# Optimization experiments

Measured on AMD Instinct MI355X. Metric: run time of the kernel, lower is better.

Reference implementation:

```python
import jax, jax.numpy as jnp
import numpy as np

B, S, D, H = 2, 2048, 1024, 16
HD = D // H


def setup_inputs() -> dict:
    key = jax.random.key(0)
    ks = jax.random.split(key, 7)
    mk = lambda k, shape, scale=1.0: (jax.random.normal(k, shape, dtype=jnp.float32) * scale)
    w_scale = 1.0 / np.sqrt(D)  # ~nn.Linear init scale
    return {
        "query": mk(ks[0], (B, S, D)),
        "key": mk(ks[1], (B, S, D)),
        "value": mk(ks[2], (B, S, D)),
        "Wq": mk(ks[3], (D, D), w_scale),
        "Wk": mk(ks[4], (D, D), w_scale),
        "Wv": mk(ks[5], (D, D), w_scale),
        "Wo": mk(ks[6], (D, D), w_scale),
    }


def reference(query, key, value, Wq, Wk, Wv, Wo):
    # torch nn.Linear(bias=False): y = x @ W.T, W is (out, in)
    def proj(x, W):
        y = jnp.einsum('bsd,ed->bse', x, W)          # [B, S, D]
        return y.reshape(x.shape[0], x.shape[1], H, HD).transpose(0, 2, 1, 3)  # [B, H, S, HD]

    Q = proj(query, Wq)
    K = proj(key, Wk)
    V = proj(value, Wv)

    # NOTE: original scales by sqrt(embedding_size), not sqrt(head_dim)
    scale = 1.0 / jnp.sqrt(jnp.asarray(D, dtype=Q.dtype))
    scores = jnp.einsum('bhqd,bhkd->bhqk', Q, K) * scale   # [B, H, Q, K]
    attn = jax.nn.softmax(scores, axis=-1)
    ctx = jnp.einsum('bhqk,bhkd->bhqd', attn, V)           # [B, H, Q, HD]
    ctx = ctx.transpose(0, 2, 1, 3).reshape(query.shape[0], query.shape[1], D)
    return jnp.einsum('bsd,ed->bse', ctx, Wo)
```

## Files before the change

### kernel.cpp

```cpp
#include <hip/hip_runtime.h>
#include <hip/hip_bf16.h>


typedef __bf16 bf16x8 __attribute__((ext_vector_type(8)));
typedef float f32x2 __attribute__((ext_vector_type(2)));
typedef float f32x4 __attribute__((ext_vector_type(4)));
typedef float f32x8 __attribute__((ext_vector_type(8)));
typedef float f32x16 __attribute__((ext_vector_type(16)));
typedef int i32x4 __attribute__((ext_vector_type(4)));

static constexpr int Bb = 2, Ss = 2048, Dd = 1024, Hh = 16, HDd = 64;
static constexpr int Mtot = Bb * Ss;

__global__ __launch_bounds__(256) void cast_all(
    const float* __restrict__ a0, const float* __restrict__ a1, const float* __restrict__ a2,
    const float* __restrict__ a3, const float* __restrict__ a4, const float* __restrict__ a5,
    const float* __restrict__ a6, __hip_bfloat16* __restrict__ d0, __hip_bfloat16* __restrict__ d1,
    __hip_bfloat16* __restrict__ d2, __hip_bfloat16* __restrict__ d3,
    __hip_bfloat16* __restrict__ d4, __hip_bfloat16* __restrict__ d5,
    __hip_bfloat16* __restrict__ d6, int nact8, int nw8) {
  const float* src;
  __hip_bfloat16* dst;
  int n8;
  switch (blockIdx.y) {
    case 0: src = a0; dst = d0; n8 = nact8; break;
    case 1: src = a1; dst = d1; n8 = nact8; break;
    case 2: src = a2; dst = d2; n8 = nact8; break;
    case 3: src = a3; dst = d3; n8 = nw8; break;
    case 4: src = a4; dst = d4; n8 = nw8; break;
    case 5: src = a5; dst = d5; n8 = nw8; break;
    default: src = a6; dst = d6; n8 = nw8; break;
  }
  int i = blockIdx.x * 256 + threadIdx.x;
  if (i >= n8) return;
  const float4* s4 = (const float4*)src + (size_t)i * 2;
  float4 a = s4[0], b = s4[1];
  union { __hip_bfloat16 h[8]; int4 v; } u;
  u.h[0] = __float2bfloat16(a.x); u.h[1] = __float2bfloat16(a.y);
  u.h[2] = __float2bfloat16(a.z); u.h[3] = __float2bfloat16(a.w);
  u.h[4] = __float2bfloat16(b.x); u.h[5] = __float2bfloat16(b.y);
  u.h[6] = __float2bfloat16(b.z); u.h[7] = __float2bfloat16(b.w);
  ((int4*)dst)[i] = u.v;
}

#define BM 128
#define BK 64

__device__ __forceinline__ void gload_lds16(const void* g, void* l) {
  __builtin_amdgcn_global_load_lds((const __attribute__((address_space(1))) unsigned*)g,
                                   (__attribute__((address_space(3))) unsigned*)l, 16, 0, 0);
}

__device__ __forceinline__ void storeC(float* C, size_t idx, float v) { C[idx] = v; }
__device__ __forceinline__ void storeC(__hip_bfloat16* C, size_t idx, float v) {
  C[idx] = __float2bfloat16(v);
}

template <typename OutT, int BNT>
__device__ __forceinline__ void gemm_bt_body(const __hip_bfloat16* __restrict__ A,
                                             const __hip_bfloat16* __restrict__ Bw,
                                             OutT* __restrict__ C, int K, int N, float cscale) {
  constexpr int NTC = BNT / 32;
  __shared__ __hip_bfloat16 As[BM * BK];
  __shared__ __hip_bfloat16 Bs[BNT * BK];
  const int tid = threadIdx.x;
  const int lane = tid & 63;
  const int wid = tid >> 6;
  const int wm = (wid >> 1) * 64;
  const int wn = (wid & 1) * (BNT / 2);
  const int bm = blockIdx.x, bn = blockIdx.y;
  const int l15 = lane & 15;
  const int lhi = lane >> 4;

  f32x4 zero = {0.f, 0.f, 0.f, 0.f};
  f32x4 acc[4][NTC];
#pragma unroll
  for (int i = 0; i < 4; ++i)
#pragma unroll
    for (int j = 0; j < NTC; ++j) acc[i][j] = zero;

  const size_t abase = (size_t)(bm * BM) * K;
  const size_t bbase = (size_t)(bn * BNT) * K;

  for (int k0 = 0; k0 < K; k0 += BK) {
#pragma unroll
    for (int p = 0; p < 4; ++p) {
      int c = p * 256 + tid;
      int row = c >> 3;
      int col = (c & 7) * 8;
      gload_lds16(A + abase + (size_t)row * K + k0 + col, (char*)As + c * 16);
    }
#pragma unroll
    for (int p = 0; p < BNT / 32; ++p) {
      int c = p * 256 + tid;
      int row = c >> 3;
      int col = (c & 7) * 8;
      gload_lds16(Bw + bbase + (size_t)row * K + k0 + col, (char*)Bs + c * 16);
    }
    __syncthreads();
#pragma unroll
    for (int kk = 0; kk < 2; ++kk) {
      bf16x8 af[4], bfr[NTC];
#pragma unroll
      for (int mt = 0; mt < 4; ++mt)
        af[mt] = *(const bf16x8*)&As[(wm + mt * 16 + l15) * BK + kk * 32 + lhi * 8];
#pragma unroll
      for (int nt = 0; nt < NTC; ++nt)
        bfr[nt] = *(const bf16x8*)&Bs[(wn + nt * 16 + l15) * BK + kk * 32 + lhi * 8];
#pragma unroll
      for (int mt = 0; mt < 4; ++mt)
#pragma unroll
        for (int nt = 0; nt < NTC; ++nt)
          acc[mt][nt] = __builtin_amdgcn_mfma_f32_16x16x32_bf16(af[mt], bfr[nt], acc[mt][nt], 0, 0, 0);
    }
    __syncthreads();
  }

#pragma unroll
  for (int mt = 0; mt < 4; ++mt)
#pragma unroll
    for (int r = 0; r < 4; ++r) {
      int row = bm * BM + wm + mt * 16 + lhi * 4 + r;
#pragma unroll
      for (int nt = 0; nt < NTC; ++nt) {
        int col = bn * BNT + wn + nt * 16 + l15;
        storeC(C, (size_t)row * N + col, acc[mt][nt][r] * cscale);
      }
    }
}

__global__ __launch_bounds__(256) void qkv_proj(
    const __hip_bfloat16* __restrict__ xq, const __hip_bfloat16* __restrict__ xk,
    const __hip_bfloat16* __restrict__ xv, const __hip_bfloat16* __restrict__ wq,
    const __hip_bfloat16* __restrict__ wk, const __hip_bfloat16* __restrict__ wv,
    __hip_bfloat16* __restrict__ Qp, __hip_bfloat16* __restrict__ Kp,
    __hip_bfloat16* __restrict__ Vp) {
  const __hip_bfloat16* A;
  const __hip_bfloat16* W;
  __hip_bfloat16* C;
  float cs = 1.0f;
  if (blockIdx.z == 0) { A = xq; W = wq; C = Qp; cs = 0.04508422f; }
  else if (blockIdx.z == 1) { A = xk; W = wk; C = Kp; }
  else { A = xv; W = wv; C = Vp; }
  gemm_bt_body<__hip_bfloat16, 128>(A, W, C, Dd, Dd, cs);
}

__global__ __launch_bounds__(256) void out_proj(const __hip_bfloat16* __restrict__ ctx,
                                                const __hip_bfloat16* __restrict__ wo,
                                                float* __restrict__ out) {
  gemm_bt_body<float, 64>(ctx, wo, out, Dd, Dd, 1.0f);
}

__global__ __launch_bounds__(256) void transpose_v(const __hip_bfloat16* __restrict__ Vp,
                                                   __hip_bfloat16* __restrict__ Vt) {
  __shared__ __hip_bfloat16 T[64][72];
  const int tid = threadIdx.x;
  const int s0 = blockIdx.x * 64;
  const int bh = blockIdx.y;
  const int b = bh >> 4, h = bh & 15;
  const __hip_bfloat16* src = Vp + (size_t)b * Ss * Dd + (size_t)h * HDd;
#pragma unroll
  for (int p = 0; p < 2; ++p) {
    int id = p * 256 + tid;
    int r = id >> 3, c8 = (id & 7) * 8;
    *(int4*)&T[r][c8] = *(const int4*)(src + (size_t)(s0 + r) * Dd + c8);
  }
  __syncthreads();
#pragma unroll
  for (int p = 0; p < 2; ++p) {
    int id = p * 256 + tid;
    int d = id >> 3, s8 = (id & 7) * 8;
    union { int4 v; __hip_bfloat16 hh[8]; } u;
#pragma unroll
    for (int j = 0; j < 8; ++j) u.hh[j] = T[s8 + j][d];
    *(int4*)(Vt + ((size_t)bh * HDd + d) * Ss + s0 + s8) = u.v;
  }
}

__global__ __launch_bounds__(256, 4) void attn_kernel(const __hip_bfloat16* __restrict__ Qp,
                                                      const __hip_bfloat16* __restrict__ Kp,
                                                      const __hip_bfloat16* __restrict__ Vt,
                                                      float* __restrict__ Po,
                                                      float* __restrict__ Pl) {
  constexpr int HT = 16;
  __shared__ __align__(16) __hip_bfloat16 Ks[2][64 * 64];
  __shared__ __align__(16) __hip_bfloat16 Vs[2][64 * 64];

  const int tid = threadIdx.x;
  const int lane = tid & 63, wid = tid >> 6;
  const int l31 = lane & 31;
  const bool hih = (lane >= 32);
  const int lhi2 = hih ? 1 : 0;

  const int bid = blockIdx.x;
  const int w = (bid & 7) * 128 + (bid >> 3);
  const int bh = w >> 5;
  const int qblk = (w & 31) >> 1;
  const int half = w & 1;

  const int b = bh >> 4, h = bh & 15;
  const size_t head_off = (size_t)b * Ss * Dd + (size_t)h * HDd;
  const size_t vt_off = (size_t)bh * HDd * Ss;
  const int qrow = qblk * 128 + wid * 32 + l31;

  bf16x8 qf[4];
#pragma unroll
  for (int ksd = 0; ksd < 4; ++ksd)
    qf[ksd] = *(const bf16x8*)(Qp + head_off + (size_t)qrow * Dd + ksd * 16 + lhi2 * 8);

  float l_run = 0.f;
  f32x16 o[2];
#pragma unroll
  for (int db = 0; db < 2; ++db)
#pragma unroll
    for (int r = 0; r < 16; ++r) o[db][r] = 0.f;

  auto stage_K = [&](int buf, int kv0) {
#pragma unroll
    for (int p = 0; p < 2; ++p) {
      int c = p * 256 + tid;
      int row = c >> 3;
      int sch = (c & 7) ^ (row & 7);
      gload_lds16(Kp + head_off + (size_t)(kv0 + row) * Dd + sch * 8,
                  (char*)&Ks[buf][0] + c * 16);
    }
  };
  auto stage_V = [&](int buf, int kv0) {
#pragma unroll
    for (int p = 0; p < 2; ++p) {
      int c = p * 256 + tid;
      int row = c >> 3;
      int sch = (c & 7) ^ (row & 7);
      gload_lds16(Vt + vt_off + (size_t)row * Ss + kv0 + sch * 8,
                  (char*)&Vs[buf][0] + c * 16);
    }
  };

  const int t0 = half * HT;
  stage_K(0, (t0 + 0) * 64);
  stage_V(0, (t0 + 0) * 64);
  stage_K(1, (t0 + 1) * 64);
  stage_V(1, (t0 + 1) * 64);
  asm volatile("s_waitcnt vmcnt(4)" ::: "memory");
  __builtin_amdgcn_s_barrier();
  __builtin_amdgcn_sched_barrier(0);

  for (int t = 0; t < HT; ++t) {
    const int cur = t & 1;
    if (t > 0 && t + 1 < HT) {
      stage_K(cur ^ 1, (t0 + t + 1) * 64);
      stage_V(cur ^ 1, (t0 + t + 1) * 64);
    }

    const char* kbase = (const char*)&Ks[cur][0];
    bf16x8 kfrag[2][4];
#pragma unroll
    for (int kb = 0; kb < 2; ++kb) {
      int row = kb * 32 + l31;
#pragma unroll
      for (int ksd = 0; ksd < 4; ++ksd)
        kfrag[kb][ksd] = *(const bf16x8*)(kbase + row * 128 +
                                          (((ksd * 2 + lhi2) ^ (row & 7)) << 4));
    }
    f32x16 st[2];
#pragma unroll
    for (int kb = 0; kb < 2; ++kb)
#pragma unroll
      for (int r = 0; r < 16; ++r) st[kb][r] = 0.f;
    __builtin_amdgcn_s_setprio(1);
#pragma unroll
    for (int kb = 0; kb < 2; ++kb)
#pragma unroll
      for (int ksd = 0; ksd < 4; ++ksd)
        st[kb] = __builtin_amdgcn_mfma_f32_32x32x16_bf16(kfrag[kb][ksd], qf[ksd], st[kb], 0, 0, 0);
    __builtin_amdgcn_s_setprio(0);

#pragma unroll
    for (int kb = 0; kb < 2; ++kb)
#pragma unroll
      for (int r = 0; r < 16; ++r) st[kb][r] = exp2f(st[kb][r]);

    f32x16 s16 = st[0] + st[1];
    f32x8 s8 = __builtin_shufflevector(s16, s16, 0, 1, 2, 3, 4, 5, 6, 7) +
               __builtin_shufflevector(s16, s16, 8, 9, 10, 11, 12, 13, 14, 15);
    f32x4 s4 = __builtin_shufflevector(s8, s8, 0, 1, 2, 3) +
               __builtin_shufflevector(s8, s8, 4, 5, 6, 7);
    f32x2 s2 = __builtin_shufflevector(s4, s4, 0, 1) + __builtin_shufflevector(s4, s4, 2, 3);
    float ps = s2[0] + s2[1];
    ps += __shfl_xor(ps, 32);
    l_run += ps;

    int cpk[2][4][2];
#pragma unroll
    for (int kb = 0; kb < 2; ++kb)
#pragma unroll
      for (int g = 0; g < 4; ++g)
#pragma unroll
        for (int i = 0; i < 2; ++i) {
          int rr;
          float lo = st[kb][g * 4 + 2 * i], hi = st[kb][g * 4 + 2 * i + 1];
          asm("v_cvt_pk_bf16_f32 %0, %1, %2" : "=v"(rr) : "v"(lo), "v"(hi));
          cpk[kb][g][i] = rr;
        }

    int own[2][2][2], rcv[2][2][2];
#pragma unroll
    for (int kb = 0; kb < 2; ++kb)
#pragma unroll
      for (int m = 0; m < 2; ++m)
#pragma unroll
        for (int i = 0; i < 2; ++i) {
          int cA = cpk[kb][2 * m][i];
          int cB = cpk[kb][2 * m + 1][i];
          int pay = hih ? cA : cB;
          own[kb][m][i] = hih ? cB : cA;
          rcv[kb][m][i] = __shfl_xor(pay, 32);
        }

    if (t + 1 < HT) {
      asm volatile("s_waitcnt vmcnt(4)" ::: "memory");
    } else {
      asm volatile("s_waitcnt vmcnt(0)" ::: "memory");
    }

    const char* vbase = (const char*)&Vs[cur][0];
    bf16x8 vfrag[4][2];
#pragma unroll
    for (int ks = 0; ks < 4; ++ks)
#pragma unroll
      for (int db = 0; db < 2; ++db) {
        int row = db * 32 + l31;
        vfrag[ks][db] = *(const bf16x8*)(vbase + row * 128 +
                                         (((ks * 2 + lhi2) ^ (row & 7)) << 4));
      }
    __builtin_amdgcn_s_setprio(1);
#pragma unroll
    for (int ks = 0; ks < 4; ++ks) {
      const int kb = ks >> 1, m = ks & 1;
      int w0 = hih ? rcv[kb][m][0] : own[kb][m][0];
      int w1 = hih ? rcv[kb][m][1] : own[kb][m][1];
      int w2 = hih ? own[kb][m][0] : rcv[kb][m][0];
      int w3 = hih ? own[kb][m][1] : rcv[kb][m][1];
      i32x4 bw = {w0, w1, w2, w3};
      bf16x8 pfrag = __builtin_bit_cast(bf16x8, bw);
#pragma unroll
      for (int db = 0; db < 2; ++db)
        o[db] = __builtin_amdgcn_mfma_f32_32x32x16_bf16(vfrag[ks][db], pfrag, o[db], 0, 0, 0);
    }
    __builtin_amdgcn_s_setprio(0);

    if (t + 1 < HT) {
      asm volatile("s_waitcnt vmcnt(2)" ::: "memory");
      __builtin_amdgcn_s_barrier();
      __builtin_amdgcn_sched_barrier(0);
    }
  }

  const int qlocal = wid * 32 + l31;
  float* prow = Po + (size_t)w * (128 * 64) + (size_t)qlocal * 64;
#pragma unroll
  for (int db = 0; db < 2; ++db)
#pragma unroll
    for (int g = 0; g < 4; ++g) {
      f32x4 v4 = {o[db][g * 4 + 0], o[db][g * 4 + 1], o[db][g * 4 + 2], o[db][g * 4 + 3]};
      *(f32x4*)(prow + db * 32 + 8 * g + 4 * lhi2) = v4;
    }
  if (!hih) Pl[(size_t)w * 128 + qlocal] = l_run;
}

__global__ __launch_bounds__(256) void merge_halves(const float* __restrict__ Po,
                                                    const float* __restrict__ Pl,
                                                    __hip_bfloat16* __restrict__ ctx) {
  const int mb = blockIdx.x;
  const int bh = mb >> 4, qblk = mb & 15;
  const int b = bh >> 4, h = bh & 15;
  const int tid = threadIdx.x;
  const int q = tid >> 1;
  const int dh = (tid & 1) * 32;
  const size_t w0 = (size_t)bh * 32 + qblk * 2;
  const float* p0 = Po + w0 * (128 * 64) + (size_t)q * 64 + dh;
  const float* p1 = p0 + 128 * 64;
  float l = Pl[w0 * 128 + q] + Pl[w0 * 128 + 128 + q];
  float inv = 1.f / l;
  __hip_bfloat16* dst =
      ctx + (size_t)b * Ss * Dd + (size_t)(qblk * 128 + q) * Dd + h * HDd + dh;
#pragma unroll
  for (int j = 0; j < 32; j += 4) {
    f32x4 a = *(const f32x4*)(p0 + j);
    f32x4 c = *(const f32x4*)(p1 + j);
    f32x4 s = (a + c) * inv;
    union { uint2 v; __hip_bfloat16 hh[4]; } u;
#pragma unroll
    for (int k = 0; k < 4; ++k) u.hh[k] = __float2bfloat16(s[k]);
    *(uint2*)(dst + j) = u.v;
  }
}

extern "C" void kernel_launch(void* const* d_in, const int* in_sizes, int n_in,
                              void* d_out, int out_size, void* d_ws, size_t ws_size,
                              hipStream_t stream) {
  const float* q_f = (const float*)d_in[0];
  const float* k_f = (const float*)d_in[1];
  const float* v_f = (const float*)d_in[2];
  const float* wq_f = (const float*)d_in[3];
  const float* wk_f = (const float*)d_in[4];
  const float* wv_f = (const float*)d_in[5];
  const float* wo_f = (const float*)d_in[6];
  float* out = (float*)d_out;

  const size_t act = (size_t)Mtot * Dd;
  const size_t wsz = (size_t)Dd * Dd;
  char* ws = (char*)d_ws;

  __hip_bfloat16* Qp = (__hip_bfloat16*)ws;   ws += act * 2;
  __hip_bfloat16* Kp = (__hip_bfloat16*)ws;   ws += act * 2;
  __hip_bfloat16* Vt = (__hip_bfloat16*)ws;   ws += act * 2;
  __hip_bfloat16* ctxb = (__hip_bfloat16*)ws; ws += act * 2;
  __hip_bfloat16* wob = (__hip_bfloat16*)ws;  ws += wsz * 2;

  char* scratch = ws;
  __hip_bfloat16* qb = (__hip_bfloat16*)scratch;
  __hip_bfloat16* kb = qb + act;
  __hip_bfloat16* vb = kb + act;
  __hip_bfloat16* wqb = vb + act;
  __hip_bfloat16* wkb = wqb + wsz;
  __hip_bfloat16* wvb = wkb + wsz;
  __hip_bfloat16* Vp = wvb + wsz;

  float* Po = (float*)scratch;
  float* Pl = Po + (size_t)1024 * 128 * 64;

  dim3 gc((unsigned)(act / 8 / 256), 7);
  cast_all<<<gc, 256, 0, stream>>>(q_f, k_f, v_f, wq_f, wk_f, wv_f, wo_f, qb, kb, vb, wqb,
                                   wkb, wvb, wob, (int)(act / 8), (int)(wsz / 8));

  dim3 gq(Mtot / BM, Dd / 128, 3);
  qkv_proj<<<gq, 256, 0, stream>>>(qb, kb, vb, wqb, wkb, wvb, Qp, Kp, Vp);

  dim3 gt(Ss / 64, Bb * Hh);
  transpose_v<<<gt, 256, 0, stream>>>(Vp, Vt);

  attn_kernel<<<1024, 256, 0, stream>>>(Qp, Kp, Vt, Po, Pl);

  merge_halves<<<512, 256, 0, stream>>>(Po, Pl, ctxb);

  dim3 go(Mtot / BM, Dd / 64);
  out_proj<<<go, 256, 0, stream>>>(ctxb, wob, out);
}
```

Measured before the change: 158.8 us.

## Compute softmax row sums via MFMA with ones and use permlane32_swap

The per-row softmax denominator is now accumulated by an extra MFMA that multiplies the bf16 P fragment by a ones matrix, replacing the VALU reduction tree and cross-lane shuffle. The P-fragment half-wave exchange uses the permlane32_swap builtin when available instead of ds-based __shfl_xor pairs. This trades VALU and LDS-permute work for one more MFMA per k-step and a 16-register accumulator. The denominator is also now summed from bf16-rounded probabilities rather than fp32 ones, which makes it consistent with the numerator.

```diff
diff --git a/kernel.cpp b/kernel.cpp
--- a/kernel.cpp
+++ b/kernel.cpp
@@ -208,12 +208,16 @@
   for (int ksd = 0; ksd < 4; ++ksd)
     qf[ksd] = *(const bf16x8*)(Qp + head_off + (size_t)qrow * Dd + ksd * 16 + lhi2 * 8);
 
-  float l_run = 0.f;
-  f32x16 o[2];
+  const i32x4 onesbits = {0x3F803F80, 0x3F803F80, 0x3F803F80, 0x3F803F80};
+  const bf16x8 ones = __builtin_bit_cast(bf16x8, onesbits);
+
+  f32x16 o[2], ol;
 #pragma unroll
   for (int db = 0; db < 2; ++db)
 #pragma unroll
     for (int r = 0; r < 16; ++r) o[db][r] = 0.f;
+#pragma unroll
+  for (int r = 0; r < 16; ++r) ol[r] = 0.f;
 
   auto stage_K = [&](int buf, int kv0) {
 #pragma unroll
@@ -280,16 +284,6 @@
 #pragma unroll
       for (int r = 0; r < 16; ++r) st[kb][r] = exp2f(st[kb][r]);
 
-    f32x16 s16 = st[0] + st[1];
-    f32x8 s8 = __builtin_shufflevector(s16, s16, 0, 1, 2, 3, 4, 5, 6, 7) +
-               __builtin_shufflevector(s16, s16, 8, 9, 10, 11, 12, 13, 14, 15);
-    f32x4 s4 = __builtin_shufflevector(s8, s8, 0, 1, 2, 3) +
-               __builtin_shufflevector(s8, s8, 4, 5, 6, 7);
-    f32x2 s2 = __builtin_shufflevector(s4, s4, 0, 1) + __builtin_shufflevector(s4, s4, 2, 3);
-    float ps = s2[0] + s2[1];
-    ps += __shfl_xor(ps, 32);
-    l_run += ps;
-
     int cpk[2][4][2];
 #pragma unroll
     for (int kb = 0; kb < 2; ++kb)
@@ -303,20 +297,6 @@
           cpk[kb][g][i] = rr;
         }
 
-    int own[2][2][2], rcv[2][2][2];
-#pragma unroll
-    for (int kb = 0; kb < 2; ++kb)
-#pragma unroll
-      for (int m = 0; m < 2; ++m)
-#pragma unroll
-        for (int i = 0; i < 2; ++i) {
-          int cA = cpk[kb][2 * m][i];
-          int cB = cpk[kb][2 * m + 1][i];
-          int pay = hih ? cA : cB;
-          own[kb][m][i] = hih ? cB : cA;
-          rcv[kb][m][i] = __shfl_xor(pay, 32);
-        }
-
     if (t + 1 < HT) {
       asm volatile("s_waitcnt vmcnt(4)" ::: "memory");
     } else {
@@ -337,15 +317,36 @@
 #pragma unroll
     for (int ks = 0; ks < 4; ++ks) {
       const int kb = ks >> 1, m = ks & 1;
-      int w0 = hih ? rcv[kb][m][0] : own[kb][m][0];
-      int w1 = hih ? rcv[kb][m][1] : own[kb][m][1];
-      int w2 = hih ? own[kb][m][0] : rcv[kb][m][0];
-      int w3 = hih ? own[kb][m][1] : rcv[kb][m][1];
+      int w0, w1, w2, w3;
+#if __has_builtin(__builtin_amdgcn_permlane32_swap)
+      {
+        auto r0 = __builtin_amdgcn_permlane32_swap(cpk[kb][2 * m][0], cpk[kb][2 * m + 1][0],
+                                                   false, false);
+        auto r1 = __builtin_amdgcn_permlane32_swap(cpk[kb][2 * m][1], cpk[kb][2 * m + 1][1],
+                                                   false, false);
+        w0 = r0[0]; w2 = r0[1];
+        w1 = r1[0]; w3 = r1[1];
+      }
+#else
+      {
+        int cA0 = cpk[kb][2 * m][0], cB0 = cpk[kb][2 * m + 1][0];
+        int cA1 = cpk[kb][2 * m][1], cB1 = cpk[kb][2 * m + 1][1];
+        int pay0 = hih ? cA0 : cB0, own0 = hih ? cB0 : cA0;
+        int pay1 = hih ? cA1 : cB1, own1 = hih ? cB1 : cA1;
+        int rcv0 = __shfl_xor(pay0, 32);
+        int rcv1 = __shfl_xor(pay1, 32);
+        w0 = hih ? rcv0 : own0;
+        w1 = hih ? rcv1 : own1;
+        w2 = hih ? own0 : rcv0;
+        w3 = hih ? own1 : rcv1;
+      }
+#endif
       i32x4 bw = {w0, w1, w2, w3};
       bf16x8 pfrag = __builtin_bit_cast(bf16x8, bw);
 #pragma unroll
       for (int db = 0; db < 2; ++db)
         o[db] = __builtin_amdgcn_mfma_f32_32x32x16_bf16(vfrag[ks][db], pfrag, o[db], 0, 0, 0);
+      ol = __builtin_amdgcn_mfma_f32_32x32x16_bf16(ones, pfrag, ol, 0, 0, 0);
     }
     __builtin_amdgcn_s_setprio(0);
 
@@ -365,7 +366,7 @@
       f32x4 v4 = {o[db][g * 4 + 0], o[db][g * 4 + 1], o[db][g * 4 + 2], o[db][g * 4 + 3]};
       *(f32x4*)(prow + db * 32 + 8 * g + 4 * lhi2) = v4;
     }
-  if (!hih) Pl[(size_t)w * 128 + qlocal] = l_run;
+  if (!hih) Pl[(size_t)w * 128 + qlocal] = ol[0];
 }
 
 __global__ __launch_bounds__(256) void merge_halves(const float* __restrict__ Po,
```

Measured after the change: 158.7 us. Within noise of the previous version (-0.0%).
